# Performance work log

Hardware: AMD Instinct MI355X
Metric: run time of the kernel (lower is better)

Reference implementation:

```python
import jax, jax.numpy as jnp
import numpy as np

N, E = 100000, 400000          # nodes, edges
DRUG_DIM, OUT, H = 75, 256, 4  # atom feat dim, out_dim, heads
D = OUT // H                   # per-head dim
G = 2048                       # num graphs (pool segments)
B, CLINE_DIM = 2048, 954       # cell-line batch, gene-expr dim
EPS = 1e-5                     # BatchNorm eps


def _tconv(x, src, dst, Wq, bq, Wk, bk, Wv, bv):
    """PyG TransformerConv, root_weight=False, concat=True. x: [n, in]."""
    n = x.shape[0]
    q = (x @ Wq + bq).reshape(n, H, D)
    k = (x @ Wk + bk).reshape(n, H, D)
    v = (x @ Wv + bv).reshape(n, H, D)
    logits = (q[dst] * k[src]).sum(-1) * (1.0 / np.sqrt(D))  # [E, H]
    # scatter-softmax over incoming edges of each destination node
    m = jax.ops.segment_max(logits, dst, num_segments=n)     # [n, H]
    m = jnp.where(jnp.isfinite(m), m, 0.0)
    e = jnp.exp(logits - m[dst])
    s = jax.ops.segment_sum(e, dst, num_segments=n)
    alpha = e / (s[dst] + 1e-16)                             # [E, H]
    out = jax.ops.segment_sum(alpha[:, :, None] * v[src], dst, num_segments=n)
    return out.reshape(n, OUT)


def _bn(x, g, b):
    mu = x.mean(0)
    var = x.var(0)  # biased, as torch BatchNorm1d in training
    return (x - mu) * jax.lax.rsqrt(var + EPS) * g + b


def setup_inputs() -> dict:
    key = jax.random.key(0)
    ks = jax.random.split(key, 16)

    def xav(k, i, o):
        return jax.random.normal(k, (i, o), jnp.float32) * np.sqrt(2.0 / (i + o))

    z = lambda: jnp.zeros((OUT,), jnp.float32)
    o = lambda: jnp.ones((OUT,), jnp.float32)
    return {
        "drug_x": jax.random.normal(ks[0], (N, DRUG_DIM), jnp.float32),
        "drug_adj": jax.random.randint(ks[1], (2, E), 0, N),
        "ibatch": jnp.sort(jax.random.randint(ks[2], (N,), 0, G)),
        "cline_x": jax.random.normal(ks[3], (B, CLINE_DIM), jnp.float32),
        "Wq1": xav(ks[4], DRUG_DIM, OUT), "bq1": z(),
        "Wk1": xav(ks[5], DRUG_DIM, OUT), "bk1": z(),
        "Wv1": xav(ks[6], DRUG_DIM, OUT), "bv1": z(),
        "g1": o(), "be1": z(),
        "Wq2": xav(ks[7], OUT, OUT), "bq2": z(),
        "Wk2": xav(ks[8], OUT, OUT), "bk2": z(),
        "Wv2": xav(ks[9], OUT, OUT), "bv2": z(),
        "g2": o(), "be2": z(),
        "Wc1": xav(ks[10], CLINE_DIM, OUT), "bc1": z(),
        "gc": o(), "bec": z(),
        "Wc2": xav(ks[11], OUT, OUT), "bc2": z(),
    }


def reference(drug_x, drug_adj, ibatch, cline_x,
              Wq1, bq1, Wk1, bk1, Wv1, bv1, g1, be1,
              Wq2, bq2, Wk2, bk2, Wv2, bv2, g2, be2,
              Wc1, bc1, gc, bec, Wc2, bc2):
    src, dst = drug_adj[0], drug_adj[1]
    # drug branch: TransformerConv -> ReLU -> BN, then residual same-layer
    h = _bn(jax.nn.relu(_tconv(drug_x, src, dst, Wq1, bq1, Wk1, bk1, Wv1, bv1)), g1, be1)
    h = h + _bn(jax.nn.relu(_tconv(h, src, dst, Wq2, bq2, Wk2, bk2, Wv2, bv2)), g2, be2)
    # global mean pool by graph id
    counts = jax.ops.segment_sum(jnp.ones((N,), h.dtype), ibatch, num_segments=G)
    pooled = jax.ops.segment_sum(h, ibatch, num_segments=G) / jnp.maximum(counts, 1.0)[:, None]
    # cline branch: Linear+Tanh, then residual (BN -> Linear -> ReLU)
    c = jnp.tanh(cline_x @ Wc1 + bc1)
    c = c + jax.nn.relu(_bn(c, gc, bec) @ Wc2 + bc2)
    return pooled, c
```

## Files before the change

### kernel.cpp

```cpp
#include <hip/hip_runtime.h>
#include <hip/hip_bf16.h>

static constexpr int N_NODES  = 100000;
static constexpr int N_EDGES  = 400000;
static constexpr int DRUG_DIM = 75;
static constexpr int OUT_C    = 256;
static constexpr int N_GRAPH  = 2048;
static constexpr int B_CL     = 2048;
static constexpr int CLINE_DIM= 954;

using bf16 = __hip_bfloat16;
using short8 = __attribute__((ext_vector_type(8))) short;
using f32x4  = __attribute__((ext_vector_type(4))) float;

template<class A, class B> struct is_same_t { static constexpr bool v = false; };
template<class A> struct is_same_t<A, A>   { static constexpr bool v = true;  };

__device__ __forceinline__ float ldf(const float* p) { return *p; }
__device__ __forceinline__ float ldf(const bf16* p)  { return __bfloat162float(*p); }
__device__ __forceinline__ void  stf(float* p, float v) { *p = v; }
__device__ __forceinline__ void  stf(bf16* p, float v)  { *p = __float2bfloat16(v); }
__device__ __forceinline__ float bfu(unsigned short u) { return __uint_as_float(((unsigned)u) << 16); }
__device__ __forceinline__ unsigned short f2bu(float f) {
    bf16 h = __float2bfloat16(f);
    return *reinterpret_cast<unsigned short*>(&h);
}

__device__ __forceinline__ void gload_lds16(const void* g, void* l) {
    __builtin_amdgcn_global_load_lds(
        (const __attribute__((address_space(1))) void*)g,
        (__attribute__((address_space(3))) void*)l, 16, 0, 0);
}

__global__ __launch_bounds__(256)
void convert_a_kernel(const float* __restrict__ A, bf16* __restrict__ Ab,
                      int K, int Kpad, int total)
{
    int idx = blockIdx.x * 256 + threadIdx.x;
    if (idx >= total) return;
    int r = idx / Kpad, k = idx - r * Kpad;
    float f = (k < K) ? A[(size_t)r * K + k] : 0.f;
    Ab[idx] = __float2bfloat16(f);
}

struct WtJob  { const float* W; bf16* Wt; int K; int n0; int Kpad; };
struct WtJobs { WtJob j[8]; };
__global__ __launch_bounds__(256)
void convert_wt8_kernel(WtJobs jobs)
{
    WtJob jb = jobs.j[blockIdx.y];
    int n = blockIdx.x;
    for (int k = threadIdx.x; k < jb.Kpad; k += 256) {
        float f = (k < jb.K) ? jb.W[(size_t)k * 256 + n] : 0.f;
        jb.Wt[(size_t)(jb.n0 + n) * jb.Kpad + k] = __float2bfloat16(f);
    }
}

__global__ __launch_bounds__(256)
void concat3_kernel(const float* __restrict__ a, const float* __restrict__ b,
                    const float* __restrict__ c, float* __restrict__ out)
{
    int i = blockIdx.x * 256 + threadIdx.x;
    if (i < 256)      out[i] = a[i];
    else if (i < 512) out[i] = b[i - 256];
    else if (i < 768) out[i] = c[i - 512];
}

template<int ACT, typename TO>
__global__ __launch_bounds__(256)
void mfma_gemm_kernel(const bf16* __restrict__ A, const bf16* __restrict__ Wt,
                      const float* __restrict__ bias, const bf16* __restrict__ res,
                      TO* __restrict__ C, int M, int K, size_t PS,
                      int NTILES, int nwg)
{
    __shared__ alignas(16) short As[128 * 64];
    __shared__ alignas(16) short Bs[128 * 64];

    const int id  = blockIdx.x;
    const int qq  = nwg >> 3, rr = nwg & 7;
    const int xcd = id & 7, loc = id >> 3;
    const int wgid = (xcd < rr ? xcd * (qq + 1) : rr * (qq + 1) + (xcd - rr) * qq) + loc;
    const int ntile = wgid % NTILES, mtile = wgid / NTILES;

    const int tid = threadIdx.x;
    const int lane = tid & 63, wid = tid >> 6;
    const int wr = wid >> 1, wc = wid & 1;

    f32x4 acc[4][4] = {};

    for (int k0 = 0; k0 < K; k0 += 64) {
        #pragma unroll
        for (int i = 0; i < 4; ++i) {
            const int chunk = i * 4 + wid;
            const int row   = chunk * 8 + (lane >> 3);
            const int e     = ((lane & 7) ^ (row & 7)) << 3;
            if (mtile * 128 + chunk * 8 + 8 <= M)
                gload_lds16(A + (size_t)(mtile * 128 + row) * K + k0 + e,
                            &As[chunk * 512]);
            gload_lds16(Wt + (size_t)(ntile * 128 + row) * K + k0 + e,
                        &Bs[chunk * 512]);
        }
        __syncthreads();
        #pragma unroll
        for (int kk = 0; kk < 2; ++kk) {
            const int coff = (kk * 32 + (lane >> 4) * 8) ^ ((lane & 7) << 3);
            short8 a[4], b[4];
            #pragma unroll
            for (int m = 0; m < 4; ++m)
                a[m] = *reinterpret_cast<const short8*>(
                    &As[(wr * 64 + m * 16 + (lane & 15)) * 64 + coff]);
            #pragma unroll
            for (int n = 0; n < 4; ++n)
                b[n] = *reinterpret_cast<const short8*>(
                    &Bs[(wc * 64 + n * 16 + (lane & 15)) * 64 + coff]);
            #pragma unroll
            for (int m = 0; m < 4; ++m)
                #pragma unroll
                for (int n = 0; n < 4; ++n)
                    acc[m][n] = __builtin_amdgcn_mfma_f32_16x16x32_bf16(
                        a[m], b[n], acc[m][n], 0, 0, 0);
        }
        __syncthreads();
    }

    TO* Cp = C + (size_t)(ntile >> 1) * PS;
    const int colbase = (ntile & 1) * 128;
    if constexpr (is_same_t<TO, bf16>::v) {
        short* eb = (wid < 2 ? As : Bs) + (wid & 1) * 4096;
        #pragma unroll
        for (int m = 0; m < 4; ++m)
            #pragma unroll
            for (int n = 0; n < 4; ++n) {
                int col_l = n * 16 + (lane & 15);
                float bcol = bias[ntile * 128 + wc * 64 + col_l];
                #pragma unroll
                for (int r = 0; r < 4; ++r) {
                    int row_l = m * 16 + ((lane >> 4) << 2) + r;
                    float val = acc[m][n][r] + bcol;
                    if (ACT == 1) val = tanhf(val);
                    if (ACT == 2) val = fmaxf(val, 0.f);
                    eb[row_l * 64 + (col_l ^ ((row_l & 7) << 3))] = (short)f2bu(val);
                }
            }
        #pragma unroll
        for (int i = 0; i < 8; ++i) {
            int row_l = i * 8 + (lane >> 3);
            int row_g = mtile * 128 + wr * 64 + row_l;
            short8 vr = *reinterpret_cast<const short8*>(
                &eb[row_l * 64 + ((((lane & 7) << 3)) ^ ((row_l & 7) << 3))]);
            if (row_g < M)
                *reinterpret_cast<short8*>(
                    &Cp[(size_t)row_g * 256 + colbase + wc * 64 + ((lane & 7) << 3)]) = vr;
        }
    } else {
        #pragma unroll
        for (int m = 0; m < 4; ++m) {
            int row0 = mtile * 128 + wr * 64 + m * 16 + ((lane >> 4) << 2);
            #pragma unroll
            for (int n = 0; n < 4; ++n) {
                int col_l = wc * 64 + n * 16 + (lane & 15);
                float bcol = bias[ntile * 128 + col_l];
                #pragma unroll
                for (int r = 0; r < 4; ++r) {
                    int row = row0 + r;
                    if (row < M) {
                        float val = acc[m][n][r] + bcol;
                        if (ACT == 1) val = tanhf(val);
                        if (ACT == 2) val = fmaxf(val, 0.f);
                        if (res) val += ldf(&res[(size_t)row * 256 + colbase + col_l]);
                        stf(&Cp[(size_t)row * 256 + colbase + col_l], val);
                    }
                }
            }
        }
    }
}

__global__ __launch_bounds__(256)
void hist_kernel(const int* __restrict__ dst, int* __restrict__ deg, int E)
{
    int e = blockIdx.x * 256 + threadIdx.x;
    if (e < E) atomicAdd(&deg[dst[e]], 1);
}

__global__ __launch_bounds__(256)
void scan1_kernel(const int* __restrict__ deg, int* __restrict__ part,
                  int* __restrict__ bsum, int n)
{
    __shared__ int sh[256];
    const int t = threadIdx.x;
    const int b0 = blockIdx.x * 1024;
    int v[4]; int s = 0;
    #pragma unroll
    for (int j = 0; j < 4; ++j) {
        int idx = b0 + t * 4 + j;
        v[j] = (idx < n) ? deg[idx] : 0;
        s += v[j];
    }
    sh[t] = s; __syncthreads();
    for (int off = 1; off < 256; off <<= 1) {
        int x = (t >= off) ? sh[t - off] : 0;
        __syncthreads();
        sh[t] += x;
        __syncthreads();
    }
    if (t == 255) bsum[blockIdx.x] = sh[255];
    int run = sh[t] - s;
    #pragma unroll
    for (int j = 0; j < 4; ++j) {
        int idx = b0 + t * 4 + j;
        if (idx < n) part[idx] = run;
        run += v[j];
    }
}

__global__ __launch_bounds__(256)
void scan2_kernel(const int* __restrict__ bsum, int* __restrict__ bsume, int nb)
{
    __shared__ int sh[256];
    const int t = threadIdx.x;
    int x0 = (t < nb) ? bsum[t] : 0;
    sh[t] = x0; __syncthreads();
    for (int off = 1; off < 256; off <<= 1) {
        int x = (t >= off) ? sh[t - off] : 0;
        __syncthreads();
        sh[t] += x;
        __syncthreads();
    }
    if (t < nb) bsume[t] = sh[t] - x0;
}

__global__ __launch_bounds__(256)
void scan3_kernel(int* __restrict__ rowptr, int* __restrict__ cursor,
                  const int* __restrict__ bsume, int n, int E)
{
    int idx = blockIdx.x * 256 + threadIdx.x;
    if (idx < n) {
        int val = rowptr[idx] + bsume[idx >> 10];
        rowptr[idx] = val;
        cursor[idx] = val;
    }
    if (idx == 0) rowptr[n] = E;
}

__global__ __launch_bounds__(256)
void scatter_kernel(const int* __restrict__ src, const int* __restrict__ dst,
                    int* __restrict__ cursor, int* __restrict__ esrc, int E)
{
    int e = blockIdx.x * 256 + threadIdx.x;
    if (e < E) {
        int slot = atomicAdd(&cursor[dst[e]], 1);
        esrc[slot] = src[e];
    }
}

__global__ __launch_bounds__(256)
void attn_fused_kernel(const int* __restrict__ rowptr, const int* __restrict__ esrc,
                       const bf16* __restrict__ q, const bf16* __restrict__ k,
                       const bf16* __restrict__ v, bf16* __restrict__ out,
                       float* __restrict__ stats, int n)
{
    __shared__ float red[8][256];
    const int lane = threadIdx.x & 63;
    const int wid  = threadIdx.x >> 6;

    float cs0 = 0.f, cs1 = 0.f, cs2 = 0.f, cs3 = 0.f;
    float cq0 = 0.f, cq1 = 0.f, cq2 = 0.f, cq3 = 0.f;

    const int stride = gridDim.x * 4;
    for (int node = blockIdx.x * 4 + wid; node < n; node += stride) {
        int lo = rowptr[node], hi = rowptr[node + 1];

        ushort4 qu = ((const ushort4*)(q + (size_t)node * 256))[lane];
        float q0 = bfu(qu.x), q1 = bfu(qu.y), q2 = bfu(qu.z), q3 = bfu(qu.w);

        float m = -INFINITY, s = 0.f;
        float a0 = 0.f, a1 = 0.f, a2 = 0.f, a3 = 0.f;

        auto upd = [&](float l, ushort4 vu) {
            if (l > m) {
                float sc = __expf(m - l);
                a0 *= sc; a1 *= sc; a2 *= sc; a3 *= sc; s *= sc;
                m = l;
            }
            float e = __expf(l - m);
            a0 = fmaf(e, bfu(vu.x), a0);
            a1 = fmaf(e, bfu(vu.y), a1);
            a2 = fmaf(e, bfu(vu.z), a2);
            a3 = fmaf(e, bfu(vu.w), a3);
            s += e;
        };

        int i = lo;
        for (; i + 2 <= hi; i += 2) {
            int sn0 = esrc[i], sn1 = esrc[i + 1];
            ushort4 ku0 = ((const ushort4*)(k + (size_t)sn0 * 256))[lane];
            ushort4 vu0 = ((const ushort4*)(v + (size_t)sn0 * 256))[lane];
            ushort4 ku1 = ((const ushort4*)(k + (size_t)sn1 * 256))[lane];
            ushort4 vu1 = ((const ushort4*)(v + (size_t)sn1 * 256))[lane];
            float p0 = q0 * bfu(ku0.x);
            p0 = fmaf(q1, bfu(ku0.y), p0);
            p0 = fmaf(q2, bfu(ku0.z), p0);
            p0 = fmaf(q3, bfu(ku0.w), p0);
            float p1 = q0 * bfu(ku1.x);
            p1 = fmaf(q1, bfu(ku1.y), p1);
            p1 = fmaf(q2, bfu(ku1.z), p1);
            p1 = fmaf(q3, bfu(ku1.w), p1);
            p0 += __shfl_xor(p0, 1);  p1 += __shfl_xor(p1, 1);
            p0 += __shfl_xor(p0, 2);  p1 += __shfl_xor(p1, 2);
            p0 += __shfl_xor(p0, 4);  p1 += __shfl_xor(p1, 4);
            p0 += __shfl_xor(p0, 8);  p1 += __shfl_xor(p1, 8);
            upd(p0 * 0.125f, vu0);
            upd(p1 * 0.125f, vu1);
        }
        if (i < hi) {
            int sn = esrc[i];
            ushort4 ku = ((const ushort4*)(k + (size_t)sn * 256))[lane];
            ushort4 vu = ((const ushort4*)(v + (size_t)sn * 256))[lane];
            float p = q0 * bfu(ku.x);
            p = fmaf(q1, bfu(ku.y), p);
            p = fmaf(q2, bfu(ku.z), p);
            p = fmaf(q3, bfu(ku.w), p);
            p += __shfl_xor(p, 1);
            p += __shfl_xor(p, 2);
            p += __shfl_xor(p, 4);
            p += __shfl_xor(p, 8);
            upd(p * 0.125f, vu);
        }

        float inv = 1.f / (s + 1e-16f);
        ushort4 o;
        o.x = f2bu(fmaxf(a0 * inv, 0.f));
        o.y = f2bu(fmaxf(a1 * inv, 0.f));
        o.z = f2bu(fmaxf(a2 * inv, 0.f));
        o.w = f2bu(fmaxf(a3 * inv, 0.f));
        ((ushort4*)(out + (size_t)node * 256))[lane] = o;

        float r0 = bfu(o.x), r1 = bfu(o.y), r2 = bfu(o.z), r3 = bfu(o.w);
        cs0 += r0; cq0 += r0 * r0;
        cs1 += r1; cq1 += r1 * r1;
        cs2 += r2; cq2 += r2 * r2;
        cs3 += r3; cq3 += r3 * r3;
    }

    red[wid][lane * 4 + 0] = cs0;  red[wid + 4][lane * 4 + 0] = cq0;
    red[wid][lane * 4 + 1] = cs1;  red[wid + 4][lane * 4 + 1] = cq1;
    red[wid][lane * 4 + 2] = cs2;  red[wid + 4][lane * 4 + 2] = cq2;
    red[wid][lane * 4 + 3] = cs3;  red[wid + 4][lane * 4 + 3] = cq3;
    __syncthreads();
    int t = threadIdx.x;
    float ssum = red[0][t] + red[1][t] + red[2][t] + red[3][t];
    float sqq  = red[4][t] + red[5][t] + red[6][t] + red[7][t];
    float* sl = stats + (size_t)(blockIdx.x & 7) * 512;
    atomicAdd(&sl[t], ssum);
    atomicAdd(&sl[256 + t], sqq);
}

template<typename TX>
__global__ __launch_bounds__(256)
void col_stats_kernel(const TX* __restrict__ x, float* __restrict__ stats, int M)
{
    const int c = threadIdx.x;
    const int r0 = blockIdx.x * 64;
    const int r1 = min(r0 + 64, M);
    float ls = 0.f, lq = 0.f;
    for (int r = r0; r < r1; ++r) {
        float val = ldf(&x[(size_t)r * 256 + c]);
        ls += val;
        lq += val * val;
    }
    atomicAdd(&stats[c], ls);
    atomicAdd(&stats[256 + c], lq);
}

__global__ __launch_bounds__(256)
void bn_fold_kernel(bf16* __restrict__ Wt, const float* __restrict__ bin,
                    float* __restrict__ bout, const float* __restrict__ stats,
                    const float* __restrict__ g, const float* __restrict__ be,
                    float* __restrict__ s_out, float* __restrict__ t_out, float invM)
{
    __shared__ float sh[256];
    const int n = blockIdx.x, k = threadIdx.x;
    float sum = 0.f, sq = 0.f;
    #pragma unroll
    for (int s = 0; s < 8; ++s) {
        sum += stats[s * 512 + k];
        sq  += stats[s * 512 + 256 + k];
    }
    float mu  = sum * invM;
    float var = sq * invM - mu * mu;
    float scale = g[k] * rsqrtf(var + 1e-5f);
    float shift = be[k] - mu * scale;
    float w = ldf(&Wt[(size_t)n * 256 + k]);
    Wt[(size_t)n * 256 + k] = __float2bfloat16(w * scale);
    sh[k] = shift * w;
    __syncthreads();
    for (int off = 128; off; off >>= 1) {
        if (k < off) sh[k] += sh[k + off];
        __syncthreads();
    }
    if (k == 0) bout[n] = bin[n] + sh[0];
    if (s_out && n == 0) { s_out[k] = scale; t_out[k] = shift; }
}

__global__ __launch_bounds__(256)
void pool_bn_kernel(const bf16* __restrict__ a2, const bf16* __restrict__ h1,
                    const int* __restrict__ ibatch, const float* __restrict__ stats,
                    const float* __restrict__ g2, const float* __restrict__ be2,
                    const float* __restrict__ s1, const float* __restrict__ t1,
                    float* __restrict__ out, float invM)
{
    int g = blockIdx.x;
    __shared__ int bounds[2];
    if (threadIdx.x == 0) {
        int lo = 0, hi = N_NODES;
        while (lo < hi) { int mid = (lo + hi) >> 1; if (ibatch[mid] < g) lo = mid + 1; else hi = mid; }
        bounds[0] = lo;
        int lo2 = lo, hi2 = N_NODES;
        while (lo2 < hi2) { int mid = (lo2 + hi2) >> 1; if (ibatch[mid] < g + 1) lo2 = mid + 1; else hi2 = mid; }
        bounds[1] = lo2;
    }
    __syncthreads();
    int lo = bounds[0], hi = bounds[1];
    int c = threadIdx.x;
    float sa = 0.f, sh = 0.f;
    for (int r = lo; r < hi; ++r) {
        sa += ldf(&a2[(size_t)r * 256 + c]);
        sh += ldf(&h1[(size_t)r * 256 + c]);
    }
    float sum = 0.f, sq = 0.f;
    #pragma unroll
    for (int s = 0; s < 8; ++s) {
        sum += stats[s * 512 + c];
        sq  += stats[s * 512 + 256 + c];
    }
    float mu  = sum * invM;
    float var = sq * invM - mu * mu;
    float sc2 = g2[c] * rsqrtf(var + 1e-5f);
    float sh2 = be2[c] - mu * sc2;
    int cnt = hi - lo;
    out[(size_t)g * 256 + c] =
        (cnt > 0) ? (sc2 * sa + s1[c] * sh) / cnt + sh2 + t1[c] : 0.f;
}

extern "C" void kernel_launch(void* const* d_in, const int* in_sizes, int n_in,
                              void* d_out, int out_size, void* d_ws, size_t ws_size,
                              hipStream_t stream)
{
    const float* drug_x  = (const float*)d_in[0];
    const int*   adj     = (const int*)  d_in[1];
    const int*   ibatch  = (const int*)  d_in[2];
    const float* cline_x = (const float*)d_in[3];
    const float* Wq1 = (const float*)d_in[4];  const float* bq1 = (const float*)d_in[5];
    const float* Wk1 = (const float*)d_in[6];  const float* bk1 = (const float*)d_in[7];
    const float* Wv1 = (const float*)d_in[8];  const float* bv1 = (const float*)d_in[9];
    const float* g1  = (const float*)d_in[10]; const float* be1 = (const float*)d_in[11];
    const float* Wq2 = (const float*)d_in[12]; const float* bq2 = (const float*)d_in[13];
    const float* Wk2 = (const float*)d_in[14]; const float* bk2 = (const float*)d_in[15];
    const float* Wv2 = (const float*)d_in[16]; const float* bv2 = (const float*)d_in[17];
    const float* g2  = (const float*)d_in[18]; const float* be2 = (const float*)d_in[19];
    const float* Wc1 = (const float*)d_in[20]; const float* bc1 = (const float*)d_in[21];
    const float* gc  = (const float*)d_in[22]; const float* bec = (const float*)d_in[23];
    const float* Wc2 = (const float*)d_in[24]; const float* bc2 = (const float*)d_in[25];

    const int* srcp = adj;
    const int* dstp = adj + N_EDGES;

    char* p = (char*)d_ws;
    auto take = [&p](size_t bytes) {
        char* r = p;
        p += (bytes + 15) & ~(size_t)15;
        return r;
    };
    const size_t PS = (size_t)N_NODES * 256;
    bf16*  qkv   = (bf16*)take(PS * 3 * sizeof(bf16));
    bf16*  h1    = (bf16*)take(PS * sizeof(bf16));
    int*   rowptr= (int*)take((size_t)(N_NODES + 1) * sizeof(int));
    int*   degcur= (int*)take((size_t)N_NODES * sizeof(int));
    int*   bsum  = (int*)take(256 * sizeof(int));
    int*   bsume = (int*)take(256 * sizeof(int));
    int*   esrc  = (int*)take((size_t)N_EDGES * sizeof(int));
    float* stats = (float*)take(8 * 512 * sizeof(float));
    float* s1buf = (float*)take(256 * sizeof(float));
    float* t1buf = (float*)take(256 * sizeof(float));
    bf16*  Wt1   = (bf16*)take((size_t)768 * 128 * sizeof(bf16));
    bf16*  Wt2   = (bf16*)take((size_t)768 * 256 * sizeof(bf16));
    bf16*  Wtc1  = (bf16*)take((size_t)256 * 960 * sizeof(bf16));
    bf16*  Wtc2  = (bf16*)take((size_t)256 * 256 * sizeof(bf16));
    float* bc2f  = (float*)take(256 * sizeof(float));
    float* bias1 = (float*)take(768 * sizeof(float));
    float* bias2 = (float*)take(768 * sizeof(float));
    size_t needed = (size_t)(p - (char*)d_ws);
    if (ws_size < needed) return;

    bf16* drug_xb  = h1;
    bf16* cline_xb = qkv;
    bf16* c1b      = qkv + (size_t)2048 * 960;

    bf16* qpl = qkv;
    bf16* kpl = qkv + PS;
    bf16* vpl = qkv + 2 * PS;

    float* out_pool = (float*)d_out;
    float* out_c    = out_pool + (size_t)N_GRAPH * OUT_C;

    const int MT_N = (N_NODES + 127) / 128;
    const int nwgN = 6 * MT_N;
    const int nwgB = 2 * (B_CL / 128);

    convert_a_kernel<<<(N_NODES * 128 + 255) / 256, 256, 0, stream>>>(
        drug_x, drug_xb, DRUG_DIM, 128, N_NODES * 128);
    WtJobs jobs = {{
        { Wq1, Wt1, DRUG_DIM,   0, 128 },
        { Wk1, Wt1, DRUG_DIM, 256, 128 },
        { Wv1, Wt1, DRUG_DIM, 512, 128 },
        { Wq2, Wt2, 256,        0, 256 },
        { Wk2, Wt2, 256,      256, 256 },
        { Wv2, Wt2, 256,      512, 256 },
        { Wc1, Wtc1, CLINE_DIM, 0, 960 },
        { Wc2, Wtc2, 256,       0, 256 },
    }};
    convert_wt8_kernel<<<dim3(256, 8), 256, 0, stream>>>(jobs);
    concat3_kernel<<<3, 256, 0, stream>>>(bq1, bk1, bv1, bias1);
    concat3_kernel<<<3, 256, 0, stream>>>(bq2, bk2, bv2, bias2);

    hipMemsetAsync(degcur, 0, N_NODES * sizeof(int), stream);
    hist_kernel<<<(N_EDGES + 255) / 256, 256, 0, stream>>>(dstp, degcur, N_EDGES);
    const int NB1 = (N_NODES + 1023) / 1024;
    scan1_kernel<<<NB1, 256, 0, stream>>>(degcur, rowptr, bsum, N_NODES);
    scan2_kernel<<<1, 256, 0, stream>>>(bsum, bsume, NB1);
    scan3_kernel<<<(N_NODES + 255) / 256, 256, 0, stream>>>(rowptr, degcur, bsume, N_NODES, N_EDGES);
    scatter_kernel<<<(N_EDGES + 255) / 256, 256, 0, stream>>>(srcp, dstp, degcur, esrc, N_EDGES);

    mfma_gemm_kernel<0, bf16><<<nwgN, 256, 0, stream>>>(
        drug_xb, Wt1, bias1, nullptr, qkv, N_NODES, 128, PS, 6, nwgN);
    hipMemsetAsync(stats, 0, 8 * 512 * sizeof(float), stream);
    attn_fused_kernel<<<4096, 256, 0, stream>>>(rowptr, esrc, qpl, kpl, vpl, h1,
                                                stats, N_NODES);
    bn_fold_kernel<<<768, 256, 0, stream>>>(Wt2, bias2, bias2, stats,
                                            g1, be1, s1buf, t1buf, 1.0f / N_NODES);

    mfma_gemm_kernel<0, bf16><<<nwgN, 256, 0, stream>>>(
        h1, Wt2, bias2, nullptr, qkv, N_NODES, 256, PS, 6, nwgN);
    hipMemsetAsync(stats, 0, 8 * 512 * sizeof(float), stream);
    attn_fused_kernel<<<4096, 256, 0, stream>>>(rowptr, esrc, qpl, kpl, vpl, qpl,
                                                stats, N_NODES);
    pool_bn_kernel<<<N_GRAPH, 256, 0, stream>>>(qpl, h1, ibatch, stats,
                                                g2, be2, s1buf, t1buf, out_pool,
                                                1.0f / N_NODES);

    convert_a_kernel<<<(B_CL * 960 + 255) / 256, 256, 0, stream>>>(
        cline_x, cline_xb, CLINE_DIM, 960, B_CL * 960);
    mfma_gemm_kernel<1, bf16><<<nwgB, 256, 0, stream>>>(
        cline_xb, Wtc1, bc1, nullptr, c1b, B_CL, 960, 0, 2, nwgB);
    hipMemsetAsync(stats, 0, 8 * 512 * sizeof(float), stream);
    col_stats_kernel<bf16><<<(B_CL + 63) / 64, 256, 0, stream>>>(c1b, stats, B_CL);
    bn_fold_kernel<<<256, 256, 0, stream>>>(Wtc2, bc2, bc2f, stats,
                                            gc, bec, nullptr, nullptr, 1.0f / B_CL);
    mfma_gemm_kernel<2, float><<<nwgB, 256, 0, stream>>>(
        c1b, Wtc2, bc2f, c1b, out_c, B_CL, 256, 0, 2, nwgB);
}
```

Measured before the change: 471.9 us.

## Merge cell-line branch launches into the drug-branch kernels via job dispatch

```diff
diff --git a/kernel.cpp b/kernel.cpp
--- a/kernel.cpp
+++ b/kernel.cpp
@@ -12,9 +12,6 @@
 using bf16 = __hip_bfloat16;
 using short8 = __attribute__((ext_vector_type(8))) short;
 using f32x4  = __attribute__((ext_vector_type(4))) float;
-
-template<class A, class B> struct is_same_t { static constexpr bool v = false; };
-template<class A> struct is_same_t<A, A>   { static constexpr bool v = true;  };
 
 __device__ __forceinline__ float ldf(const float* p) { return *p; }
 __device__ __forceinline__ float ldf(const bf16* p)  { return __bfloat162float(*p); }
@@ -33,14 +30,22 @@
 }
 
 __global__ __launch_bounds__(256)
-void convert_a_kernel(const float* __restrict__ A, bf16* __restrict__ Ab,
-                      int K, int Kpad, int total)
-{
-    int idx = blockIdx.x * 256 + threadIdx.x;
-    if (idx >= total) return;
-    int r = idx / Kpad, k = idx - r * Kpad;
-    float f = (k < K) ? A[(size_t)r * K + k] : 0.f;
-    Ab[idx] = __float2bfloat16(f);
+void convert_a2_kernel(const float* __restrict__ A0, bf16* __restrict__ O0,
+                       int K0, int Kp0, int t0, int nb0,
+                       const float* __restrict__ A1, bf16* __restrict__ O1,
+                       int K1, int Kp1, int t1)
+{
+    if ((int)blockIdx.x < nb0) {
+        int idx = blockIdx.x * 256 + threadIdx.x;
+        if (idx >= t0) return;
+        int r = idx / Kp0, k = idx - r * Kp0;
+        O0[idx] = __float2bfloat16((k < K0) ? A0[(size_t)r * K0 + k] : 0.f);
+    } else {
+        int idx = (blockIdx.x - nb0) * 256 + threadIdx.x;
+        if (idx >= t1) return;
+        int r = idx / Kp1, k = idx - r * Kp1;
+        O1[idx] = __float2bfloat16((k < K1) ? A1[(size_t)r * K1 + k] : 0.f);
+    }
 }
 
 struct WtJob  { const float* W; bf16* Wt; int K; int n0; int Kpad; };
@@ -66,21 +71,25 @@
     else if (i < 768) out[i] = c[i - 512];
 }
 
-template<int ACT, typename TO>
-__global__ __launch_bounds__(256)
-void mfma_gemm_kernel(const bf16* __restrict__ A, const bf16* __restrict__ Wt,
-                      const float* __restrict__ bias, const bf16* __restrict__ res,
-                      TO* __restrict__ C, int M, int K, size_t PS,
-                      int NTILES, int nwg)
+struct GemmJob {
+    const bf16* A; const bf16* Wt; const float* bias; const bf16* res;
+    char* C; size_t PS; int M, K, NTILES, nwg, act, out_f32;
+};
+__global__ __launch_bounds__(256)
+void mfma_gemm2_kernel(GemmJob jA, GemmJob jB, int nwgTot)
 {
     __shared__ alignas(16) short As[128 * 64];
     __shared__ alignas(16) short Bs[128 * 64];
 
     const int id  = blockIdx.x;
-    const int qq  = nwg >> 3, rr = nwg & 7;
+    const int qq  = nwgTot >> 3, rr = nwgTot & 7;
     const int xcd = id & 7, loc = id >> 3;
-    const int wgid = (xcd < rr ? xcd * (qq + 1) : rr * (qq + 1) + (xcd - rr) * qq) + loc;
-    const int ntile = wgid % NTILES, mtile = wgid / NTILES;
+    int wgid = (xcd < rr ? xcd * (qq + 1) : rr * (qq + 1) + (xcd - rr) * qq) + loc;
+
+    GemmJob J = (wgid < jA.nwg) ? jA : jB;
+    if (wgid >= jA.nwg) wgid -= jA.nwg;
+    const int ntile = wgid % J.NTILES, mtile = wgid / J.NTILES;
+    const int M = J.M, K = J.K;
 
     const int tid = threadIdx.x;
     const int lane = tid & 63, wid = tid >> 6;
@@ -95,9 +104,9 @@
             const int row   = chunk * 8 + (lane >> 3);
             const int e     = ((lane & 7) ^ (row & 7)) << 3;
             if (mtile * 128 + chunk * 8 + 8 <= M)
-                gload_lds16(A + (size_t)(mtile * 128 + row) * K + k0 + e,
+                gload_lds16(J.A + (size_t)(mtile * 128 + row) * K + k0 + e,
                             &As[chunk * 512]);
-            gload_lds16(Wt + (size_t)(ntile * 128 + row) * K + k0 + e,
+            gload_lds16(J.Wt + (size_t)(ntile * 128 + row) * K + k0 + e,
                         &Bs[chunk * 512]);
         }
         __syncthreads();
@@ -123,22 +132,22 @@
         __syncthreads();
     }
 
-    TO* Cp = C + (size_t)(ntile >> 1) * PS;
     const int colbase = (ntile & 1) * 128;
-    if constexpr (is_same_t<TO, bf16>::v) {
+    if (!J.out_f32) {
+        bf16* Cp = (bf16*)J.C + (size_t)(ntile >> 1) * J.PS;
         short* eb = (wid < 2 ? As : Bs) + (wid & 1) * 4096;
         #pragma unroll
         for (int m = 0; m < 4; ++m)
             #pragma unroll
             for (int n = 0; n < 4; ++n) {
                 int col_l = n * 16 + (lane & 15);
-                float bcol = bias[ntile * 128 + wc * 64 + col_l];
+                float bcol = J.bias[ntile * 128 + wc * 64 + col_l];
                 #pragma unroll
                 for (int r = 0; r < 4; ++r) {
                     int row_l = m * 16 + ((lane >> 4) << 2) + r;
                     float val = acc[m][n][r] + bcol;
-                    if (ACT == 1) val = tanhf(val);
-                    if (ACT == 2) val = fmaxf(val, 0.f);
+                    if (J.act == 1) val = tanhf(val);
+                    if (J.act == 2) val = fmaxf(val, 0.f);
                     eb[row_l * 64 + (col_l ^ ((row_l & 7) << 3))] = (short)f2bu(val);
                 }
             }
@@ -153,21 +162,22 @@
                     &Cp[(size_t)row_g * 256 + colbase + wc * 64 + ((lane & 7) << 3)]) = vr;
         }
     } else {
+        float* Cp = (float*)J.C + (size_t)(ntile >> 1) * J.PS;
         #pragma unroll
         for (int m = 0; m < 4; ++m) {
             int row0 = mtile * 128 + wr * 64 + m * 16 + ((lane >> 4) << 2);
             #pragma unroll
             for (int n = 0; n < 4; ++n) {
                 int col_l = wc * 64 + n * 16 + (lane & 15);
-                float bcol = bias[ntile * 128 + col_l];
+                float bcol = J.bias[ntile * 128 + col_l];
                 #pragma unroll
                 for (int r = 0; r < 4; ++r) {
                     int row = row0 + r;
                     if (row < M) {
                         float val = acc[m][n][r] + bcol;
-                        if (ACT == 1) val = tanhf(val);
-                        if (ACT == 2) val = fmaxf(val, 0.f);
-                        if (res) val += ldf(&res[(size_t)row * 256 + colbase + col_l]);
+                        if (J.act == 1) val = tanhf(val);
+                        if (J.act == 2) val = fmaxf(val, 0.f);
+                        if (J.res) val += ldf(&J.res[(size_t)row * 256 + colbase + col_l]);
                         stf(&Cp[(size_t)row * 256 + colbase + col_l], val);
                     }
                 }
@@ -356,9 +366,8 @@
     atomicAdd(&sl[256 + t], sqq);
 }
 
-template<typename TX>
-__global__ __launch_bounds__(256)
-void col_stats_kernel(const TX* __restrict__ x, float* __restrict__ stats, int M)
+__global__ __launch_bounds__(256)
+void col_stats_kernel(const bf16* __restrict__ x, float* __restrict__ stats, int M)
 {
     const int c = threadIdx.x;
     const int r0 = blockIdx.x * 64;
@@ -373,34 +382,38 @@
     atomicAdd(&stats[256 + c], lq);
 }
 
-__global__ __launch_bounds__(256)
-void bn_fold_kernel(bf16* __restrict__ Wt, const float* __restrict__ bin,
-                    float* __restrict__ bout, const float* __restrict__ stats,
-                    const float* __restrict__ g, const float* __restrict__ be,
-                    float* __restrict__ s_out, float* __restrict__ t_out, float invM)
+struct FoldJob {
+    bf16* Wt; const float* bin; float* bout; const float* stats;
+    const float* g; const float* be; float* s_out; float* t_out; float invM;
+};
+__global__ __launch_bounds__(256)
+void bn_fold2_kernel(FoldJob a, FoldJob b, int nA)
 {
     __shared__ float sh[256];
-    const int n = blockIdx.x, k = threadIdx.x;
+    const bool isA = ((int)blockIdx.x < nA);
+    FoldJob J = isA ? a : b;
+    const int n = isA ? blockIdx.x : blockIdx.x - nA;
+    const int k = threadIdx.x;
     float sum = 0.f, sq = 0.f;
     #pragma unroll
     for (int s = 0; s < 8; ++s) {
-        sum += stats[s * 512 + k];
-        sq  += stats[s * 512 + 256 + k];
-    }
-    float mu  = sum * invM;
-    float var = sq * invM - mu * mu;
-    float scale = g[k] * rsqrtf(var + 1e-5f);
-    float shift = be[k] - mu * scale;
-    float w = ldf(&Wt[(size_t)n * 256 + k]);
-    Wt[(size_t)n * 256 + k] = __float2bfloat16(w * scale);
+        sum += J.stats[s * 512 + k];
+        sq  += J.stats[s * 512 + 256 + k];
+    }
+    float mu  = sum * J.invM;
+    float var = sq * J.invM - mu * mu;
+    float scale = J.g[k] * rsqrtf(var + 1e-5f);
+    float shift = J.be[k] - mu * scale;
+    float w = ldf(&J.Wt[(size_t)n * 256 + k]);
+    J.Wt[(size_t)n * 256 + k] = __float2bfloat16(w * scale);
     sh[k] = shift * w;
     __syncthreads();
     for (int off = 128; off; off >>= 1) {
         if (k < off) sh[k] += sh[k + off];
         __syncthreads();
     }
-    if (k == 0) bout[n] = bin[n] + sh[0];
-    if (s_out && n == 0) { s_out[k] = scale; t_out[k] = shift; }
+    if (k == 0) J.bout[n] = J.bin[n] + sh[0];
+    if (J.s_out && n == 0) { J.s_out[k] = scale; J.t_out[k] = shift; }
 }
 
 __global__ __launch_bounds__(256)
@@ -475,12 +488,15 @@
     const size_t PS = (size_t)N_NODES * 256;
     bf16*  qkv   = (bf16*)take(PS * 3 * sizeof(bf16));
     bf16*  h1    = (bf16*)take(PS * sizeof(bf16));
+    bf16*  cline_xb = (bf16*)take((size_t)B_CL * 960 * sizeof(bf16));
+    bf16*  c1b   = (bf16*)take((size_t)B_CL * 256 * sizeof(bf16));
     int*   rowptr= (int*)take((size_t)(N_NODES + 1) * sizeof(int));
     int*   degcur= (int*)take((size_t)N_NODES * sizeof(int));
     int*   bsum  = (int*)take(256 * sizeof(int));
     int*   bsume = (int*)take(256 * sizeof(int));
     int*   esrc  = (int*)take((size_t)N_EDGES * sizeof(int));
     float* stats = (float*)take(8 * 512 * sizeof(float));
+    float* statsC= (float*)take(8 * 512 * sizeof(float));
     float* s1buf = (float*)take(256 * sizeof(float));
     float* t1buf = (float*)take(256 * sizeof(float));
     bf16*  Wt1   = (bf16*)take((size_t)768 * 128 * sizeof(bf16));
@@ -493,10 +509,7 @@
     size_t needed = (size_t)(p - (char*)d_ws);
     if (ws_size < needed) return;
 
-    bf16* drug_xb  = h1;
-    bf16* cline_xb = qkv;
-    bf16* c1b      = qkv + (size_t)2048 * 960;
-
+    bf16* drug_xb = h1;
     bf16* qpl = qkv;
     bf16* kpl = qkv + PS;
     bf16* vpl = qkv + 2 * PS;
@@ -508,8 +521,11 @@
     const int nwgN = 6 * MT_N;
     const int nwgB = 2 * (B_CL / 128);
 
-    convert_a_kernel<<<(N_NODES * 128 + 255) / 256, 256, 0, stream>>>(
-        drug_x, drug_xb, DRUG_DIM, 128, N_NODES * 128);
+    const int nb_drug = (N_NODES * 128 + 255) / 256;
+    const int nb_cl   = (B_CL * 960 + 255) / 256;
+    convert_a2_kernel<<<nb_drug + nb_cl, 256, 0, stream>>>(
+        drug_x, drug_xb, DRUG_DIM, 128, N_NODES * 128, nb_drug,
+        cline_x, cline_xb, CLINE_DIM, 960, B_CL * 960);
     WtJobs jobs = {{
         { Wq1, Wt1, DRUG_DIM,   0, 128 },
         { Wk1, Wt1, DRUG_DIM, 256, 128 },
@@ -531,32 +547,29 @@
     scan2_kernel<<<1, 256, 0, stream>>>(bsum, bsume, NB1);
     scan3_kernel<<<(N_NODES + 255) / 256, 256, 0, stream>>>(rowptr, degcur, bsume, N_NODES, N_EDGES);
     scatter_kernel<<<(N_EDGES + 255) / 256, 256, 0, stream>>>(srcp, dstp, degcur, esrc, N_EDGES);
-
-    mfma_gemm_kernel<0, bf16><<<nwgN, 256, 0, stream>>>(
-        drug_xb, Wt1, bias1, nullptr, qkv, N_NODES, 128, PS, 6, nwgN);
-    hipMemsetAsync(stats, 0, 8 * 512 * sizeof(float), stream);
+    hipMemsetAsync(stats, 0, 2 * 8 * 512 * sizeof(float), stream);
+
+    GemmJob jDrug1 = { drug_xb, Wt1, bias1, nullptr, (char*)qkv, PS,
+                       N_NODES, 128, 6, nwgN, 0, 0 };
+    GemmJob jCl1   = { cline_xb, Wtc1, bc1, nullptr, (char*)c1b, 0,
+                       B_CL, 960, 2, nwgB, 1, 0 };
+    mfma_gemm2_kernel<<<nwgN + nwgB, 256, 0, stream>>>(jDrug1, jCl1, nwgN + nwgB);
     attn_fused_kernel<<<4096, 256, 0, stream>>>(rowptr, esrc, qpl, kpl, vpl, h1,
                                                 stats, N_NODES);
-    bn_fold_kernel<<<768, 256, 0, stream>>>(Wt2, bias2, bias2, stats,
-                                            g1, be1, s1buf, t1buf, 1.0f / N_NODES);
-
-    mfma_gemm_kernel<0, bf16><<<nwgN, 256, 0, stream>>>(
-        h1, Wt2, bias2, nullptr, qkv, N_NODES, 256, PS, 6, nwgN);
+    col_stats_kernel<<<(B_CL + 63) / 64, 256, 0, stream>>>(c1b, statsC, B_CL);
+    FoldJob fDrug = { Wt2, bias2, bias2, stats, g1, be1, s1buf, t1buf, 1.0f / N_NODES };
+    FoldJob fCl   = { Wtc2, bc2, bc2f, statsC, gc, bec, nullptr, nullptr, 1.0f / B_CL };
+    bn_fold2_kernel<<<768 + 256, 256, 0, stream>>>(fDrug, fCl, 768);
+
+    GemmJob jDrug2 = { h1, Wt2, bias2, nullptr, (char*)qkv, PS,
+                       N_NODES, 256, 6, nwgN, 0, 0 };
+    GemmJob jCl2   = { c1b, Wtc2, bc2f, c1b, (char*)out_c, 0,
+                       B_CL, 256, 2, nwgB, 2, 1 };
+    mfma_gemm2_kernel<<<nwgN + nwgB, 256, 0, stream>>>(jDrug2, jCl2, nwgN + nwgB);
     hipMemsetAsync(stats, 0, 8 * 512 * sizeof(float), stream);
     attn_fused_kernel<<<4096, 256, 0, stream>>>(rowptr, esrc, qpl, kpl, vpl, qpl,
                                                 stats, N_NODES);
     pool_bn_kernel<<<N_GRAPH, 256, 0, stream>>>(qpl, h1, ibatch, stats,
                                                 g2, be2, s1buf, t1buf, out_pool,
                                                 1.0f / N_NODES);
-
-    convert_a_kernel<<<(B_CL * 960 + 255) / 256, 256, 0, stream>>>(
-        cline_x, cline_xb, CLINE_DIM, 960, B_CL * 960);
-    mfma_gemm_kernel<1, bf16><<<nwgB, 256, 0, stream>>>(
-        cline_xb, Wtc1, bc1, nullptr, c1b, B_CL, 960, 0, 2, nwgB);
-    hipMemsetAsync(stats, 0, 8 * 512 * sizeof(float), stream);
-    col_stats_kernel<bf16><<<(B_CL + 63) / 64, 256, 0, stream>>>(c1b, stats, B_CL);
-    bn_fold_kernel<<<256, 256, 0, stream>>>(Wtc2, bc2, bc2f, stats,
-                                            gc, bec, nullptr, nullptr, 1.0f / B_CL);
-    mfma_gemm_kernel<2, float><<<nwgB, 256, 0, stream>>>(
-        c1b, Wtc2, bc2f, c1b, out_c, B_CL, 256, 0, 2, nwgB);
-}
+}
```

Result: faster. 457.1 us (-3.1%).
